# Performance work log

Measured on AMD Instinct MI355X. Metric: run time of the kernel, lower is better.

## Reference

```python
import jax, jax.numpy as jnp
import numpy as np

N = 50000   # num_embs = num nodes
E = 800000  # num edges
D = 256     # feature dim
L = 4       # num layers
EPS = 1e-5


def setup_inputs() -> dict:
    key = jax.random.key(0)
    ks = jax.random.split(key, 8)
    scale = 1.0 / np.sqrt(D)
    return {
        "x": jax.random.normal(ks[0], (N, D), dtype=jnp.float32),  # ignored by forward
        "edge_index": jax.random.randint(ks[1], (2, E), 0, N, dtype=jnp.int32),
        "edge_weight": jax.random.uniform(ks[2], (E,), dtype=jnp.float32),
        "emb_weight": jax.random.normal(ks[3], (N, D), dtype=jnp.float32),
        "ln_w": jnp.ones((L, D), dtype=jnp.float32),
        "ln_b": jnp.zeros((L, D), dtype=jnp.float32),
        "conv_w": jax.random.normal(ks[4], (L, D, D), dtype=jnp.float32) * scale,
        "conv_b": jnp.zeros((L, D), dtype=jnp.float32),
        "post_w": jax.random.normal(ks[5], (D, D), dtype=jnp.float32) * scale,
        "post_b": jnp.zeros((D,), dtype=jnp.float32),
    }


def _layer_norm(h, w, b):
    mu = jnp.mean(h, axis=-1, keepdims=True)
    var = jnp.mean(jnp.square(h - mu), axis=-1, keepdims=True)
    return (h - mu) * jax.lax.rsqrt(var + EPS) * w + b


def reference(x, edge_index, edge_weight, emb_weight, ln_w, ln_b, conv_w, conv_b, post_w, post_b):
    # GCNConv semantics (PyG defaults): add self-loops (weight 1), symmetric norm.
    loop = jnp.arange(N, dtype=edge_index.dtype)
    src = jnp.concatenate([edge_index[0], loop])
    dst = jnp.concatenate([edge_index[1], loop])
    w = jnp.concatenate([edge_weight, jnp.ones((N,), edge_weight.dtype)])
    deg = jax.ops.segment_sum(w, dst, num_segments=N)
    dinv = jnp.where(deg > 0, jax.lax.rsqrt(jnp.maximum(deg, 1e-12)), 0.0)
    coef = (dinv[src] * w * dinv[dst])[:, None]  # [E+N, 1]

    h = emb_weight  # forward ignores x; cond_emb is None
    for i in range(L):
        z = _layer_norm(h, ln_w[i], ln_b[i])          # node LayerNorm
        zw = z @ conv_w[i]                             # linear transform
        agg = jax.ops.segment_sum(coef * zw[src], dst, num_segments=N)
        z = agg + conv_b[i]
        z = jax.nn.gelu(z, approximate=False)          # torch GELU is exact
        h = z + h                                      # residual (dropout=0)
    return h @ post_w + post_b
```

## Files before the change

### kernel.cpp

```cpp
#include <hip/hip_runtime.h>
#include <hip/hip_bf16.h>

#define N_NODES 50000
#define N_EDGES 800000
#define DIM     256
#define NLAYERS 4
#define EPS     1e-5f
#define SCAN_B  196
#define MASK40  ((1ULL << 40) - 1)
#define EPACK_CAP (N_EDGES + 15 * N_NODES + 32)
#define STRIDE  260

typedef __bf16 bf16x8 __attribute__((ext_vector_type(8)));
typedef float  f32x4  __attribute__((ext_vector_type(4)));
typedef float  f32x2  __attribute__((ext_vector_type(2)));
typedef unsigned short u16x8 __attribute__((ext_vector_type(8)));
typedef unsigned short u16x4 __attribute__((ext_vector_type(4)));
typedef int            i32x4 __attribute__((ext_vector_type(4)));
typedef unsigned int   u32x2 __attribute__((ext_vector_type(2)));

__device__ __forceinline__ unsigned short f2b(float f) {
    __hip_bfloat16 h = __float2bfloat16(f);
    return __builtin_bit_cast(unsigned short, h);
}
__device__ __forceinline__ float b2f(unsigned short u) {
    unsigned int v = ((unsigned int)u) << 16;
    return __builtin_bit_cast(float, v);
}
__device__ __forceinline__ float gelu_exact(float x) {
    return 0.5f * x * (1.0f + erff(x * 0.70710678118654752f));
}
__device__ __forceinline__ unsigned int pack_fp8x4(float a, float b, float c, float d) {
    int v = 0;
    v = __builtin_amdgcn_cvt_pk_fp8_f32(a, b, v, false);
    v = __builtin_amdgcn_cvt_pk_fp8_f32(c, d, v, true);
    return (unsigned int)v;
}

__global__ __launch_bounds__(256) void hist_kernel(const int* __restrict__ dst,
                                                   const float* __restrict__ w,
                                                   unsigned long long* __restrict__ cnt64,
                                                   int* __restrict__ rank) {
    int e = blockIdx.x * 256 + threadIdx.x;
    if (e >= N_EDGES) return;
    int d = dst[e];
    unsigned long long wfix = (unsigned long long)(w[e] * 4294967296.0f);
    unsigned long long old = atomicAdd(&cnt64[d], (1ULL << 40) | wfix);
    rank[e] = (int)(old >> 40);
}

__global__ __launch_bounds__(256) void scan_a_kernel(const unsigned long long* __restrict__ cnt64,
                                                     float* __restrict__ dinv,
                                                     int* __restrict__ bsum) {
    __shared__ int l[256];
    int i = blockIdx.x * 256 + threadIdx.x;
    int pc = 0;
    if (i < N_NODES) {
        unsigned long long v = cnt64[i];
        int cnt = (int)(v >> 40);
        float sw = (float)(v & MASK40) * 2.3283064365386963e-10f;
        dinv[i] = rsqrtf(1.0f + sw);
        pc = (cnt + 15) & ~15;
    }
    l[threadIdx.x] = pc;
    __syncthreads();
    for (int o = 128; o > 0; o >>= 1) {
        if (threadIdx.x < o) l[threadIdx.x] += l[threadIdx.x + o];
        __syncthreads();
    }
    if (threadIdx.x == 0) bsum[blockIdx.x] = l[0];
}

__global__ __launch_bounds__(256) void scan_b_kernel(const int* __restrict__ bsum,
                                                     int* __restrict__ boff,
                                                     int* __restrict__ rowptr) {
    __shared__ int l[256];
    int t = threadIdx.x;
    l[t] = (t < SCAN_B) ? bsum[t] : 0;
    __syncthreads();
    if (t == 0) {
        int run = 0;
        for (int j = 0; j < SCAN_B; ++j) { int v = l[j]; l[j] = run; run += v; }
        rowptr[N_NODES] = run;
    }
    __syncthreads();
    boff[t] = l[t];
}

__global__ __launch_bounds__(256) void scan_c_kernel(const unsigned long long* __restrict__ cnt64,
                                                     const int* __restrict__ boff,
                                                     int* __restrict__ rowptr) {
    __shared__ int l[256];
    int i = blockIdx.x * 256 + threadIdx.x;
    int pc = 0;
    if (i < N_NODES) {
        int cnt = (int)(cnt64[i] >> 40);
        pc = (cnt + 15) & ~15;
    }
    l[threadIdx.x] = pc;
    __syncthreads();
    if (threadIdx.x == 0) {
        int run = 0;
        for (int j = 0; j < 256; ++j) { int v = l[j]; l[j] = run; run += v; }
    }
    __syncthreads();
    if (i < N_NODES) rowptr[i] = boff[blockIdx.x] + l[threadIdx.x];
}

__global__ __launch_bounds__(256) void fill_kernel(const int* __restrict__ src,
                                                   const int* __restrict__ dst,
                                                   const float* __restrict__ w,
                                                   const float* __restrict__ dinv,
                                                   const int* __restrict__ rowptr,
                                                   const int* __restrict__ rank,
                                                   int2* __restrict__ epack) {
    int e = blockIdx.x * 256 + threadIdx.x;
    if (e >= N_EDGES) return;
    int s = src[e], d = dst[e];
    float c = dinv[s] * w[e] * dinv[d];
    int p = rowptr[d] + rank[e];
    epack[p] = make_int2(s << 8, __float_as_int(c));
}

__global__ __launch_bounds__(256) void convw_kernel(const float* __restrict__ conv_w,
                                                    const float* __restrict__ post_w,
                                                    unsigned short* __restrict__ Wt) {
    int idx = blockIdx.x * 256 + threadIdx.x;
    if (idx >= 5 * 65536) return;
    int m = idx >> 16;
    int r = idx & 65535;
    int n = r >> 8;
    int k = r & 255;
    float v = (m < 4) ? conv_w[m * 65536 + k * 256 + n] : post_w[k * 256 + n];
    Wt[idx] = f2b(v);
}

__global__ __launch_bounds__(256) void ln_cast_kernel(const float* __restrict__ H,
                                                      const float* __restrict__ lnw,
                                                      const float* __restrict__ lnb,
                                                      unsigned char* __restrict__ Z8,
                                                      unsigned short* __restrict__ Hbf) {
    int row = blockIdx.x * 4 + (threadIdx.x >> 6);
    int lane = threadIdx.x & 63;
    const float4 x = *(const float4*)(H + (size_t)row * DIM + lane * 4);
    float s = x.x + x.y + x.z + x.w;
    for (int o = 32; o > 0; o >>= 1) s += __shfl_xor(s, o);
    float mu = s * (1.0f / DIM);
    float d0 = x.x - mu, d1 = x.y - mu, d2 = x.z - mu, d3 = x.w - mu;
    float v = d0 * d0 + d1 * d1 + d2 * d2 + d3 * d3;
    for (int o = 32; o > 0; o >>= 1) v += __shfl_xor(v, o);
    float rs = rsqrtf(v * (1.0f / DIM) + EPS);
    const float4 ww = *(const float4*)(lnw + lane * 4);
    const float4 bb = *(const float4*)(lnb + lane * 4);
    float z0 = d0 * rs * ww.x + bb.x;
    float z1 = d1 * rs * ww.y + bb.y;
    float z2 = d2 * rs * ww.z + bb.z;
    float z3 = d3 * rs * ww.w + bb.w;
    *(unsigned int*)(Z8 + (size_t)row * DIM + lane * 4) = pack_fp8x4(z0, z1, z2, z3);
    ushort4 h4;
    h4.x = f2b(x.x); h4.y = f2b(x.y); h4.z = f2b(x.z); h4.w = f2b(x.w);
    *(ushort4*)(Hbf + (size_t)row * DIM + lane * 4) = h4;
}

__global__ __launch_bounds__(256) void agg_kernel(const unsigned char* __restrict__ Z8,
                                                  const int* __restrict__ rowptr,
                                                  const int2* __restrict__ epack,
                                                  const float* __restrict__ dinv,
                                                  unsigned short* __restrict__ AGG) {
    int node = blockIdx.x * 4 + (threadIdx.x >> 6);
    int lane = threadIdx.x & 63;
    int g = lane >> 5;
    int colB = (lane & 31) * 8;

    float di = dinv[node];
    float scg = (g == 0) ? di * di : 0.0f;
    const u32x2 zs = *(const u32x2*)(Z8 + (size_t)node * DIM + colB);
    f32x2 a0, a1, a2, a3;
    {
        f32x2 p0 = __builtin_amdgcn_cvt_pk_f32_fp8(zs[0], false);
        f32x2 p1 = __builtin_amdgcn_cvt_pk_f32_fp8(zs[0], true);
        f32x2 p2 = __builtin_amdgcn_cvt_pk_f32_fp8(zs[1], false);
        f32x2 p3 = __builtin_amdgcn_cvt_pk_f32_fp8(zs[1], true);
        a0 = scg * p0; a1 = scg * p1; a2 = scg * p2; a3 = scg * p3;
    }

    int e0 = rowptr[node], e1 = rowptr[node + 1];
    for (int e = e0; e < e1; e += 16) {
        const int2* pp = epack + e + 8 * g;
        const i32x4 q0 = *(const i32x4*)pp;
        const i32x4 q1 = *(const i32x4*)(pp + 2);
        const i32x4 q2 = *(const i32x4*)(pp + 4);
        const i32x4 q3 = *(const i32x4*)(pp + 6);
        const u32x2 v0 = *(const u32x2*)(Z8 + q0[0] + colB);
        const u32x2 v1 = *(const u32x2*)(Z8 + q0[2] + colB);
        const u32x2 v2 = *(const u32x2*)(Z8 + q1[0] + colB);
        const u32x2 v3 = *(const u32x2*)(Z8 + q1[2] + colB);
        const u32x2 v4 = *(const u32x2*)(Z8 + q2[0] + colB);
        const u32x2 v5 = *(const u32x2*)(Z8 + q2[2] + colB);
        const u32x2 v6 = *(const u32x2*)(Z8 + q3[0] + colB);
        const u32x2 v7 = *(const u32x2*)(Z8 + q3[2] + colB);
        float c0 = __int_as_float(q0[1]), c1 = __int_as_float(q0[3]);
        float c2 = __int_as_float(q1[1]), c3 = __int_as_float(q1[3]);
        float c4 = __int_as_float(q2[1]), c5 = __int_as_float(q2[3]);
        float c6 = __int_as_float(q3[1]), c7 = __int_as_float(q3[3]);
        #pragma unroll
        for (int h = 0; h < 8; ++h) {
            u32x2 vv; float cc;
            switch (h) {
                case 0: vv = v0; cc = c0; break;
                case 1: vv = v1; cc = c1; break;
                case 2: vv = v2; cc = c2; break;
                case 3: vv = v3; cc = c3; break;
                case 4: vv = v4; cc = c4; break;
                case 5: vv = v5; cc = c5; break;
                case 6: vv = v6; cc = c6; break;
                default: vv = v7; cc = c7; break;
            }
            f32x2 p0 = __builtin_amdgcn_cvt_pk_f32_fp8(vv[0], false);
            f32x2 p1 = __builtin_amdgcn_cvt_pk_f32_fp8(vv[0], true);
            f32x2 p2 = __builtin_amdgcn_cvt_pk_f32_fp8(vv[1], false);
            f32x2 p3 = __builtin_amdgcn_cvt_pk_f32_fp8(vv[1], true);
            a0 += cc * p0; a1 += cc * p1; a2 += cc * p2; a3 += cc * p3;
        }
    }
    float a[8] = {a0[0], a0[1], a1[0], a1[1], a2[0], a2[1], a3[0], a3[1]};
    #pragma unroll
    for (int j = 0; j < 8; ++j) a[j] += __shfl_xor(a[j], 32);

    if (g == 0) {
        u16x8 z;
        #pragma unroll
        for (int j = 0; j < 8; ++j) z[j] = f2b(a[j]);
        *(u16x8*)(AGG + (size_t)node * DIM + colB) = z;
    }
}

__global__ __launch_bounds__(256) void gemm_fused_kernel(const unsigned short* __restrict__ A,
                                                         const unsigned short* __restrict__ Bt,
                                                         const float* __restrict__ bias,
                                                         unsigned short* __restrict__ Hbf,
                                                         const float* __restrict__ lnw,
                                                         const float* __restrict__ lnb,
                                                         unsigned char* __restrict__ Z8,
                                                         int doLN) {
    __shared__ unsigned short stile[64 * STRIDE];
    int tid = threadIdx.x;
    int wave = tid >> 6;
    int lane = tid & 63;
    int q = lane >> 4;
    int c16 = lane & 15;
    int mbase = blockIdx.x * 64;
    int cbase = wave * 64;

    const unsigned short* aptr[4];
    #pragma unroll
    for (int nt = 0; nt < 4; ++nt) {
        int row = mbase + nt * 16 + c16;
        if (row >= N_NODES) row = N_NODES - 1;
        aptr[nt] = A + (size_t)row * DIM;
    }
    const unsigned short* wptr[4];
    #pragma unroll
    for (int ct = 0; ct < 4; ++ct)
        wptr[ct] = Bt + (size_t)(cbase + ct * 16 + c16) * DIM;

    f32x4 acc[4][4] = {};
    #pragma unroll 1
    for (int k0 = 0; k0 < DIM; k0 += 32) {
        bf16x8 nf[4], wf[4];
        #pragma unroll
        for (int nt = 0; nt < 4; ++nt)
            nf[nt] = __builtin_bit_cast(bf16x8, *(const u16x8*)(aptr[nt] + k0 + q * 8));
        #pragma unroll
        for (int ct = 0; ct < 4; ++ct)
            wf[ct] = __builtin_bit_cast(bf16x8, *(const u16x8*)(wptr[ct] + k0 + q * 8));
        #pragma unroll
        for (int nt = 0; nt < 4; ++nt)
            #pragma unroll
            for (int ct = 0; ct < 4; ++ct)
                acc[nt][ct] = __builtin_amdgcn_mfma_f32_16x16x32_bf16(wf[ct], nf[nt], acc[nt][ct], 0, 0, 0);
    }

    #pragma unroll
    for (int nt = 0; nt < 4; ++nt) {
        int row = nt * 16 + c16;
        #pragma unroll
        for (int ct = 0; ct < 4; ++ct) {
            int col = cbase + ct * 16 + q * 4;
            u16x4 pk;
            pk[0] = f2b(acc[nt][ct][0]);
            pk[1] = f2b(acc[nt][ct][1]);
            pk[2] = f2b(acc[nt][ct][2]);
            pk[3] = f2b(acc[nt][ct][3]);
            *(u16x4*)&stile[row * STRIDE + col] = pk;
        }
    }
    __syncthreads();

    int r  = tid >> 2;
    int ck = tid & 3;
    int node = mbase + r;
    if (node < N_NODES) {
        const int cb = ck * 64;
        float h[64];
        float psum = 0.0f, psq = 0.0f;
        #pragma unroll
        for (int i = 0; i < 8; ++i) {
            const u16x8 sv = *(const u16x8*)&stile[r * STRIDE + cb + i * 8];
            const f32x4 b0 = *(const f32x4*)(bias + cb + i * 8);
            const f32x4 b1 = *(const f32x4*)(bias + cb + i * 8 + 4);
            const u16x8 hv = *(const u16x8*)(Hbf + (size_t)node * DIM + cb + i * 8);
            #pragma unroll
            for (int j = 0; j < 8; ++j) {
                float v = b2f(sv[j]) + (j < 4 ? b0[j] : b1[j - 4]);
                float hn = gelu_exact(v) + b2f(hv[j]);
                h[i * 8 + j] = hn;
                psum += hn;
                psq += hn * hn;
            }
        }
        #pragma unroll
        for (int i = 0; i < 8; ++i) {
            u16x8 hw;
            #pragma unroll
            for (int j = 0; j < 8; ++j) hw[j] = f2b(h[i * 8 + j]);
            *(u16x8*)(Hbf + (size_t)node * DIM + cb + i * 8) = hw;
        }
        if (doLN) {
            psum += __shfl_xor(psum, 1);
            psum += __shfl_xor(psum, 2);
            psq  += __shfl_xor(psq, 1);
            psq  += __shfl_xor(psq, 2);
            float mu = psum * (1.0f / DIM);
            float var = fmaxf(psq * (1.0f / DIM) - mu * mu, 0.0f);
            float rs = rsqrtf(var + EPS);
            #pragma unroll
            for (int i2 = 0; i2 < 4; ++i2) {
                int c0 = cb + i2 * 16;
                unsigned int pk[4];
                #pragma unroll
                for (int k = 0; k < 4; ++k) {
                    const f32x4 ww = *(const f32x4*)(lnw + c0 + k * 4);
                    const f32x4 lb = *(const f32x4*)(lnb + c0 + k * 4);
                    int hb = i2 * 16 + k * 4;
                    float y0 = (h[hb + 0] - mu) * rs * ww[0] + lb[0];
                    float y1 = (h[hb + 1] - mu) * rs * ww[1] + lb[1];
                    float y2 = (h[hb + 2] - mu) * rs * ww[2] + lb[2];
                    float y3 = (h[hb + 3] - mu) * rs * ww[3] + lb[3];
                    pk[k] = pack_fp8x4(y0, y1, y2, y3);
                }
                uint4 st = make_uint4(pk[0], pk[1], pk[2], pk[3]);
                *(uint4*)(Z8 + (size_t)node * DIM + c0) = st;
            }
        }
    }
}

__global__ __launch_bounds__(256) void gemm_out_kernel(const unsigned short* __restrict__ A,
                                                       const unsigned short* __restrict__ Bt,
                                                       float* __restrict__ C,
                                                       const float* __restrict__ bias) {
    int tid = threadIdx.x;
    int wave = tid >> 6;
    int lane = tid & 63;
    int q = lane >> 4;
    int c16 = lane & 15;
    int mbase = blockIdx.x * 64;
    int cbase = wave * 64;

    const unsigned short* aptr[4];
    #pragma unroll
    for (int nt = 0; nt < 4; ++nt) {
        int row = mbase + nt * 16 + c16;
        if (row >= N_NODES) row = N_NODES - 1;
        aptr[nt] = A + (size_t)row * DIM;
    }
    const unsigned short* wptr[4];
    #pragma unroll
    for (int ct = 0; ct < 4; ++ct)
        wptr[ct] = Bt + (size_t)(cbase + ct * 16 + c16) * DIM;

    f32x4 acc[4][4] = {};
    #pragma unroll 1
    for (int k0 = 0; k0 < DIM; k0 += 32) {
        bf16x8 nf[4], wf[4];
        #pragma unroll
        for (int nt = 0; nt < 4; ++nt)
            nf[nt] = __builtin_bit_cast(bf16x8, *(const u16x8*)(aptr[nt] + k0 + q * 8));
        #pragma unroll
        for (int ct = 0; ct < 4; ++ct)
            wf[ct] = __builtin_bit_cast(bf16x8, *(const u16x8*)(wptr[ct] + k0 + q * 8));
        #pragma unroll
        for (int nt = 0; nt < 4; ++nt)
            #pragma unroll
            for (int ct = 0; ct < 4; ++ct)
                acc[nt][ct] = __builtin_amdgcn_mfma_f32_16x16x32_bf16(nf[nt], wf[ct], acc[nt][ct], 0, 0, 0);
    }

    float bb[4];
    #pragma unroll
    for (int ct = 0; ct < 4; ++ct)
        bb[ct] = bias[cbase + ct * 16 + c16];
    #pragma unroll
    for (int nt = 0; nt < 4; ++nt) {
        #pragma unroll
        for (int j = 0; j < 4; ++j) {
            int node = mbase + nt * 16 + q * 4 + j;
            if (node >= N_NODES) continue;
            #pragma unroll
            for (int ct = 0; ct < 4; ++ct) {
                int chan = cbase + ct * 16 + c16;
                C[(size_t)node * DIM + chan] = acc[nt][ct][j] + bb[ct];
            }
        }
    }
}

extern "C" void kernel_launch(void* const* d_in, const int* in_sizes, int n_in,
                              void* d_out, int out_size, void* d_ws, size_t ws_size,
                              hipStream_t stream) {
    const int*   ei     = (const int*)d_in[1];
    const int*   src    = ei;
    const int*   dst    = ei + N_EDGES;
    const float* ew     = (const float*)d_in[2];
    const float* emb    = (const float*)d_in[3];
    const float* ln_w   = (const float*)d_in[4];
    const float* ln_b   = (const float*)d_in[5];
    const float* conv_w = (const float*)d_in[6];
    const float* conv_b = (const float*)d_in[7];
    const float* post_w = (const float*)d_in[8];
    const float* post_b = (const float*)d_in[9];
    float* out = (float*)d_out;

    char* w = (char*)d_ws;
    size_t off = 0;
    auto alloc = [&](size_t bytes) -> char* {
        char* p = w + off;
        off += (bytes + 255) & ~(size_t)255;
        return p;
    };
    unsigned long long* cnt64 = (unsigned long long*)alloc((size_t)N_NODES * 8);
    float* dinv   = (float*)alloc((size_t)N_NODES * 4);
    int*   rank   = (int*)alloc((size_t)N_EDGES * 4);
    int*   rowptr = (int*)alloc((size_t)(N_NODES + 1) * 4);
    int*   bsum   = (int*)alloc(256 * 4);
    int*   boff   = (int*)alloc(256 * 4);
    int2*  epack  = (int2*)alloc((size_t)EPACK_CAP * 8);
    unsigned short* Wt    = (unsigned short*)alloc((size_t)5 * 65536 * 2);
    unsigned short* AGG16 = (unsigned short*)alloc((size_t)N_NODES * DIM * 2);
    unsigned char*  Z8    = (unsigned char*)alloc((size_t)N_NODES * DIM);
    unsigned short* Hbf   = (unsigned short*)alloc((size_t)N_NODES * DIM * 2);

    hipMemsetAsync(cnt64, 0, (size_t)N_NODES * 8, stream);
    hipMemsetAsync(epack, 0, (size_t)EPACK_CAP * 8, stream);
    hist_kernel<<<N_EDGES / 256, 256, 0, stream>>>(dst, ew, cnt64, rank);
    scan_a_kernel<<<SCAN_B, 256, 0, stream>>>(cnt64, dinv, bsum);
    scan_b_kernel<<<1, 256, 0, stream>>>(bsum, boff, rowptr);
    scan_c_kernel<<<SCAN_B, 256, 0, stream>>>(cnt64, boff, rowptr);
    fill_kernel<<<N_EDGES / 256, 256, 0, stream>>>(src, dst, ew, dinv, rowptr, rank, epack);
    convw_kernel<<<(5 * 65536) / 256, 256, 0, stream>>>(conv_w, post_w, Wt);

    const int GEMM_GRID = (N_NODES + 63) / 64;
    ln_cast_kernel<<<N_NODES / 4, 256, 0, stream>>>(emb, ln_w, ln_b, Z8, Hbf);
    for (int l = 0; l < NLAYERS; ++l) {
        agg_kernel<<<N_NODES / 4, 256, 0, stream>>>(Z8, rowptr, epack, dinv, AGG16);
        int doLN = (l < NLAYERS - 1) ? 1 : 0;
        const float* nlw = doLN ? (ln_w + (l + 1) * DIM) : ln_w;
        const float* nlb = doLN ? (ln_b + (l + 1) * DIM) : ln_b;
        gemm_fused_kernel<<<GEMM_GRID, 256, 0, stream>>>(AGG16, Wt + (size_t)l * 65536,
                                                         conv_b + (size_t)l * DIM, Hbf,
                                                         nlw, nlb, Z8, doLN);
    }
    gemm_out_kernel<<<GEMM_GRID, 256, 0, stream>>>(Hbf, Wt + (size_t)4 * 65536, out, post_b);
}
```

Baseline: 701.5 us.

## Shrink GEMM row tile to 32 with register double-buffered loads

Both GEMM kernels now process 32 rows per block instead of 64, which doubles the grid and halves the accumulator and LDS footprint. The launch bounds request 4 blocks per SM. The K loop software-pipelines its global loads by prefetching the next k-slice into registers while the MFMAs run on the current one. The epilogue is remapped to 8 threads per row, with an extra shuffle step for the LayerNorm reduction. The cost is that the weight tile is reloaded for twice as many blocks, and each block does less MFMA work to hide latency.

```diff
diff --git a/kernel.cpp b/kernel.cpp
--- a/kernel.cpp
+++ b/kernel.cpp
@@ -235,54 +235,71 @@
     }
 }
 
-__global__ __launch_bounds__(256) void gemm_fused_kernel(const unsigned short* __restrict__ A,
-                                                         const unsigned short* __restrict__ Bt,
-                                                         const float* __restrict__ bias,
-                                                         unsigned short* __restrict__ Hbf,
-                                                         const float* __restrict__ lnw,
-                                                         const float* __restrict__ lnb,
-                                                         unsigned char* __restrict__ Z8,
-                                                         int doLN) {
-    __shared__ unsigned short stile[64 * STRIDE];
+__global__ __launch_bounds__(256, 4) void gemm_fused_kernel(const unsigned short* __restrict__ A,
+                                                            const unsigned short* __restrict__ Bt,
+                                                            const float* __restrict__ bias,
+                                                            unsigned short* __restrict__ Hbf,
+                                                            const float* __restrict__ lnw,
+                                                            const float* __restrict__ lnb,
+                                                            unsigned char* __restrict__ Z8,
+                                                            int doLN) {
+    __shared__ unsigned short stile[32 * STRIDE];
     int tid = threadIdx.x;
     int wave = tid >> 6;
     int lane = tid & 63;
     int q = lane >> 4;
     int c16 = lane & 15;
-    int mbase = blockIdx.x * 64;
+    int mbase = blockIdx.x * 32;
     int cbase = wave * 64;
 
-    const unsigned short* aptr[4];
-    #pragma unroll
-    for (int nt = 0; nt < 4; ++nt) {
+    const unsigned short* aptr[2];
+    #pragma unroll
+    for (int nt = 0; nt < 2; ++nt) {
         int row = mbase + nt * 16 + c16;
         if (row >= N_NODES) row = N_NODES - 1;
-        aptr[nt] = A + (size_t)row * DIM;
+        aptr[nt] = A + (size_t)row * DIM + q * 8;
     }
     const unsigned short* wptr[4];
     #pragma unroll
     for (int ct = 0; ct < 4; ++ct)
-        wptr[ct] = Bt + (size_t)(cbase + ct * 16 + c16) * DIM;
-
-    f32x4 acc[4][4] = {};
+        wptr[ct] = Bt + (size_t)(cbase + ct * 16 + c16) * DIM + q * 8;
+
+    f32x4 acc[2][4] = {};
+    bf16x8 nfc[2], wfc[4];
+    #pragma unroll
+    for (int nt = 0; nt < 2; ++nt)
+        nfc[nt] = __builtin_bit_cast(bf16x8, *(const u16x8*)(aptr[nt]));
+    #pragma unroll
+    for (int ct = 0; ct < 4; ++ct)
+        wfc[ct] = __builtin_bit_cast(bf16x8, *(const u16x8*)(wptr[ct]));
+
     #pragma unroll 1
-    for (int k0 = 0; k0 < DIM; k0 += 32) {
-        bf16x8 nf[4], wf[4];
-        #pragma unroll
-        for (int nt = 0; nt < 4; ++nt)
-            nf[nt] = __builtin_bit_cast(bf16x8, *(const u16x8*)(aptr[nt] + k0 + q * 8));
+    for (int k0 = 32; k0 < DIM; k0 += 32) {
+        bf16x8 nfn[2], wfn[4];
+        #pragma unroll
+        for (int nt = 0; nt < 2; ++nt)
+            nfn[nt] = __builtin_bit_cast(bf16x8, *(const u16x8*)(aptr[nt] + k0));
         #pragma unroll
         for (int ct = 0; ct < 4; ++ct)
-            wf[ct] = __builtin_bit_cast(bf16x8, *(const u16x8*)(wptr[ct] + k0 + q * 8));
-        #pragma unroll
-        for (int nt = 0; nt < 4; ++nt)
+            wfn[ct] = __builtin_bit_cast(bf16x8, *(const u16x8*)(wptr[ct] + k0));
+        #pragma unroll
+        for (int nt = 0; nt < 2; ++nt)
             #pragma unroll
             for (int ct = 0; ct < 4; ++ct)
-                acc[nt][ct] = __builtin_amdgcn_mfma_f32_16x16x32_bf16(wf[ct], nf[nt], acc[nt][ct], 0, 0, 0);
-    }
-
-    #pragma unroll
-    for (int nt = 0; nt < 4; ++nt) {
+                acc[nt][ct] = __builtin_amdgcn_mfma_f32_16x16x32_bf16(wfc[ct], nfc[nt], acc[nt][ct], 0, 0, 0);
+        #pragma unroll
+        for (int nt = 0; nt < 2; ++nt) nfc[nt] = nfn[nt];
+        #pragma unroll
+        for (int ct = 0; ct < 4; ++ct) wfc[ct] = wfn[ct];
+    }
+    #pragma unroll
+    for (int nt = 0; nt < 2; ++nt)
+        #pragma unroll
+        for (int ct = 0; ct < 4; ++ct)
+            acc[nt][ct] = __builtin_amdgcn_mfma_f32_16x16x32_bf16(wfc[ct], nfc[nt], acc[nt][ct], 0, 0, 0);
+
+    #pragma unroll
+    for (int nt = 0; nt < 2; ++nt) {
         int row = nt * 16 + c16;
         #pragma unroll
         for (int ct = 0; ct < 4; ++ct) {
@@ -297,15 +314,14 @@
     }
     __syncthreads();
 
-    int r  = tid >> 2;
-    int ck = tid & 3;
+    int r  = tid >> 3;
+    int cb = (tid & 7) * 32;
     int node = mbase + r;
     if (node < N_NODES) {
-        const int cb = ck * 64;
-        float h[64];
+        float h[32];
         float psum = 0.0f, psq = 0.0f;
         #pragma unroll
-        for (int i = 0; i < 8; ++i) {
+        for (int i = 0; i < 4; ++i) {
             const u16x8 sv = *(const u16x8*)&stile[r * STRIDE + cb + i * 8];
             const f32x4 b0 = *(const f32x4*)(bias + cb + i * 8);
             const f32x4 b1 = *(const f32x4*)(bias + cb + i * 8 + 4);
@@ -320,7 +336,7 @@
             }
         }
         #pragma unroll
-        for (int i = 0; i < 8; ++i) {
+        for (int i = 0; i < 4; ++i) {
             u16x8 hw;
             #pragma unroll
             for (int j = 0; j < 8; ++j) hw[j] = f2b(h[i * 8 + j]);
@@ -329,13 +345,15 @@
         if (doLN) {
             psum += __shfl_xor(psum, 1);
             psum += __shfl_xor(psum, 2);
+            psum += __shfl_xor(psum, 4);
             psq  += __shfl_xor(psq, 1);
             psq  += __shfl_xor(psq, 2);
+            psq  += __shfl_xor(psq, 4);
             float mu = psum * (1.0f / DIM);
             float var = fmaxf(psq * (1.0f / DIM) - mu * mu, 0.0f);
             float rs = rsqrtf(var + EPS);
             #pragma unroll
-            for (int i2 = 0; i2 < 4; ++i2) {
+            for (int i2 = 0; i2 < 2; ++i2) {
                 int c0 = cb + i2 * 16;
                 unsigned int pk[4];
                 #pragma unroll
@@ -356,53 +374,70 @@
     }
 }
 
-__global__ __launch_bounds__(256) void gemm_out_kernel(const unsigned short* __restrict__ A,
-                                                       const unsigned short* __restrict__ Bt,
-                                                       float* __restrict__ C,
-                                                       const float* __restrict__ bias) {
+__global__ __launch_bounds__(256, 4) void gemm_out_kernel(const unsigned short* __restrict__ A,
+                                                          const unsigned short* __restrict__ Bt,
+                                                          float* __restrict__ C,
+                                                          const float* __restrict__ bias) {
     int tid = threadIdx.x;
     int wave = tid >> 6;
     int lane = tid & 63;
     int q = lane >> 4;
     int c16 = lane & 15;
-    int mbase = blockIdx.x * 64;
+    int mbase = blockIdx.x * 32;
     int cbase = wave * 64;
 
-    const unsigned short* aptr[4];
-    #pragma unroll
-    for (int nt = 0; nt < 4; ++nt) {
+    const unsigned short* aptr[2];
+    #pragma unroll
+    for (int nt = 0; nt < 2; ++nt) {
         int row = mbase + nt * 16 + c16;
         if (row >= N_NODES) row = N_NODES - 1;
-        aptr[nt] = A + (size_t)row * DIM;
+        aptr[nt] = A + (size_t)row * DIM + q * 8;
     }
     const unsigned short* wptr[4];
     #pragma unroll
     for (int ct = 0; ct < 4; ++ct)
-        wptr[ct] = Bt + (size_t)(cbase + ct * 16 + c16) * DIM;
-
-    f32x4 acc[4][4] = {};
+        wptr[ct] = Bt + (size_t)(cbase + ct * 16 + c16) * DIM + q * 8;
+
+    f32x4 acc[2][4] = {};
+    bf16x8 nfc[2], wfc[4];
+    #pragma unroll
+    for (int nt = 0; nt < 2; ++nt)
+        nfc[nt] = __builtin_bit_cast(bf16x8, *(const u16x8*)(aptr[nt]));
+    #pragma unroll
+    for (int ct = 0; ct < 4; ++ct)
+        wfc[ct] = __builtin_bit_cast(bf16x8, *(const u16x8*)(wptr[ct]));
+
     #pragma unroll 1
-    for (int k0 = 0; k0 < DIM; k0 += 32) {
-        bf16x8 nf[4], wf[4];
-        #pragma unroll
-        for (int nt = 0; nt < 4; ++nt)
-            nf[nt] = __builtin_bit_cast(bf16x8, *(const u16x8*)(aptr[nt] + k0 + q * 8));
+    for (int k0 = 32; k0 < DIM; k0 += 32) {
+        bf16x8 nfn[2], wfn[4];
+        #pragma unroll
+        for (int nt = 0; nt < 2; ++nt)
+            nfn[nt] = __builtin_bit_cast(bf16x8, *(const u16x8*)(aptr[nt] + k0));
         #pragma unroll
         for (int ct = 0; ct < 4; ++ct)
-            wf[ct] = __builtin_bit_cast(bf16x8, *(const u16x8*)(wptr[ct] + k0 + q * 8));
-        #pragma unroll
-        for (int nt = 0; nt < 4; ++nt)
+            wfn[ct] = __builtin_bit_cast(bf16x8, *(const u16x8*)(wptr[ct] + k0));
+        #pragma unroll
+        for (int nt = 0; nt < 2; ++nt)
             #pragma unroll
             for (int ct = 0; ct < 4; ++ct)
-                acc[nt][ct] = __builtin_amdgcn_mfma_f32_16x16x32_bf16(nf[nt], wf[ct], acc[nt][ct], 0, 0, 0);
-    }
+                acc[nt][ct] = __builtin_amdgcn_mfma_f32_16x16x32_bf16(nfc[nt], wfc[ct], acc[nt][ct], 0, 0, 0);
+        #pragma unroll
+        for (int nt = 0; nt < 2; ++nt) nfc[nt] = nfn[nt];
+        #pragma unroll
+        for (int ct = 0; ct < 4; ++ct) wfc[ct] = wfn[ct];
+    }
+    #pragma unroll
+    for (int nt = 0; nt < 2; ++nt)
+        #pragma unroll
+        for (int ct = 0; ct < 4; ++ct)
+            acc[nt][ct] = __builtin_amdgcn_mfma_f32_16x16x32_bf16(nfc[nt], wfc[ct], acc[nt][ct], 0, 0, 0);
 
     float bb[4];
     #pragma unroll
     for (int ct = 0; ct < 4; ++ct)
         bb[ct] = bias[cbase + ct * 16 + c16];
     #pragma unroll
-    for (int nt = 0; nt < 4; ++nt) {
+    for (int nt = 0; nt < 2; ++nt) {
         #pragma unroll
         for (int j = 0; j < 4; ++j) {
             int node = mbase + nt * 16 + q * 4 + j;
@@ -460,7 +495,7 @@
     fill_kernel<<<N_EDGES / 256, 256, 0, stream>>>(src, dst, ew, dinv, rowptr, rank, epack);
     convw_kernel<<<(5 * 65536) / 256, 256, 0, stream>>>(conv_w, post_w, Wt);
 
-    const int GEMM_GRID = (N_NODES + 63) / 64;
+    const int GEMM_GRID = (N_NODES + 31) / 32;
     ln_cast_kernel<<<N_NODES / 4, 256, 0, stream>>>(emb, ln_w, ln_b, Z8, Hbf);
     for (int l = 0; l < NLAYERS; ++l) {
         agg_kernel<<<N_NODES / 4, 256, 0, stream>>>(Z8, rowptr, epack, dinv, AGG16);
```

Result: faster. 653.3 us (-6.9%).
